# Performance work log

Hardware: AMD Instinct MI355X
Metric: run time of the kernel (lower is better)

## Reference

```python
import jax, jax.numpy as jnp
import numpy as np

B, P, K = 8, 2048, 30   # clouds, points per cloud, kNN neighbors
N = B * P
EPS = 1e-5


def _bn(h, g, b):
    # BatchNorm1d in training mode: batch stats over all non-feature axes (biased var)
    ax = tuple(range(h.ndim - 1))
    m = jnp.mean(h, axis=ax, keepdims=True)
    v = jnp.mean((h - m) ** 2, axis=ax, keepdims=True)
    return g * (h - m) * jax.lax.rsqrt(v + EPS) + b


def _mlp2(x, W0, b0, g0, be0, W1, b1, g1, be1):
    # Seq(Lin, ReLU, BN) x2, matching MLP([cin, 64, 64])
    h = _bn(jax.nn.relu(x @ W0 + b0), g0, be0)
    return _bn(jax.nn.relu(h @ W1 + b1), g1, be1)


def _edgeconv(f, W0, b0, g0, be0, W1, b1, g1, be1):
    # f: [B,P,C]. DynamicEdgeConv: kNN in feature space per cloud (self included,
    # as torch_cluster.knn does), message MLP([x_i, x_j - x_i]), max aggregation.
    s = jnp.sum(f * f, axis=-1)                                   # [B,P]
    d = s[:, :, None] + s[:, None, :] - 2.0 * jnp.einsum('bpc,bqc->bpq', f, f)
    idx = jax.lax.top_k(-d, K)[1]                                  # [B,P,K]
    xj = jax.vmap(lambda ff, ii: ff[ii])(f, idx)                   # [B,P,K,C]
    xi = jnp.broadcast_to(f[:, :, None, :], xj.shape)
    e = jnp.concatenate([xi, xj - xi], axis=-1)                    # [B,P,K,2C]
    return jnp.max(_mlp2(e, W0, b0, g0, be0, W1, b1, g1, be1), axis=2)


def _params():
    key = jax.random.key(1)
    cnt = [0]
    def W(shape, scale=0.05):
        cnt[0] += 1
        return jax.random.normal(jax.random.fold_in(key, cnt[0]), shape, jnp.float32) * scale
    p = {}
    for name, cin in (('c1', 12), ('c2', 128), ('c3', 128)):
        p[name + '_W0'] = W((cin, 64)); p[name + '_b0'] = jnp.zeros(64, jnp.float32)
        p[name + '_g0'] = jnp.ones(64, jnp.float32); p[name + '_be0'] = jnp.zeros(64, jnp.float32)
        p[name + '_W1'] = W((64, 64)); p[name + '_b1'] = jnp.zeros(64, jnp.float32)
        p[name + '_g1'] = jnp.ones(64, jnp.float32); p[name + '_be1'] = jnp.zeros(64, jnp.float32)
    p['l1_W'] = W((192, 1024)); p['l1_b'] = jnp.zeros(1024, jnp.float32)
    p['l1_g'] = jnp.ones(1024, jnp.float32); p['l1_be'] = jnp.zeros(1024, jnp.float32)
    p['h0_W'] = W((1024, 256)); p['h0_b'] = jnp.zeros(256, jnp.float32)
    p['h0_g'] = jnp.ones(256, jnp.float32); p['h0_be'] = jnp.zeros(256, jnp.float32)
    p['h1_W'] = W((256, 128)); p['h1_b'] = jnp.zeros(128, jnp.float32)
    p['h1_g'] = jnp.ones(128, jnp.float32); p['h1_be'] = jnp.zeros(128, jnp.float32)
    p['ho_W'] = W((128, 50)); p['ho_b'] = jnp.zeros(50, jnp.float32)
    return p


def setup_inputs():
    key = jax.random.key(0)
    kx, kp = jax.random.split(key)
    inp = {
        'x': jax.random.normal(kx, (N, 3), jnp.float32),
        'pos': jax.random.normal(kp, (N, 3), jnp.float32),
        'batch': jnp.repeat(jnp.arange(B, dtype=jnp.int32), P),  # B equal-size clouds
    }
    inp.update(_params())
    return inp


def reference(x, pos, batch,
              c1_W0, c1_b0, c1_g0, c1_be0, c1_W1, c1_b1, c1_g1, c1_be1,
              c2_W0, c2_b0, c2_g0, c2_be0, c2_W1, c2_b1, c2_g1, c2_be1,
              c3_W0, c3_b0, c3_g0, c3_be0, c3_W1, c3_b1, c3_g1, c3_be1,
              l1_W, l1_b, l1_g, l1_be,
              h0_W, h0_b, h0_g, h0_be,
              h1_W, h1_b, h1_g, h1_be,
              ho_W, ho_b):
    # batch is assumed to be B equal-sized, sorted clouds -> dense [B,P,C] layout
    f0 = jnp.concatenate([x, pos], axis=-1).reshape(B, P, 6)
    x1 = _edgeconv(f0, c1_W0, c1_b0, c1_g0, c1_be0, c1_W1, c1_b1, c1_g1, c1_be1)
    x2 = _edgeconv(x1, c2_W0, c2_b0, c2_g0, c2_be0, c2_W1, c2_b1, c2_g1, c2_be1)
    x3 = _edgeconv(x2, c3_W0, c3_b0, c3_g0, c3_be0, c3_W1, c3_b1, c3_g1, c3_be1)
    h = jnp.concatenate([x1, x2, x3], axis=-1).reshape(N, 192)
    h = _bn(jax.nn.relu(h @ l1_W + l1_b), l1_g, l1_be)
    h = _bn(jax.nn.relu(h @ h0_W + h0_b), h0_g, h0_be)   # dropout = identity (eval)
    h = _bn(jax.nn.relu(h @ h1_W + h1_b), h1_g, h1_be)
    return jax.nn.log_softmax(h @ ho_W + ho_b, axis=1)
```

## Files before the change

### kernel.cpp

```cpp
#include <hip/hip_runtime.h>
#include <hip/hip_bf16.h>
#include <stdint.h>

#define BNUM 8
#define PNUM 2048
#define KNN  30
#define KSEL 40
#define KCAP 64
#define NPT  (BNUM*PNUM)
#define EPSF 1e-5f

typedef unsigned long long u64;
typedef unsigned short ushort_t;
typedef __attribute__((ext_vector_type(8))) short short8v;
typedef __attribute__((ext_vector_type(4))) float f32x4;

__device__ __forceinline__ unsigned mono_key(float d) {
    unsigned u = __float_as_uint(d);
    return (u & 0x80000000u) ? ~u : (u | 0x80000000u);
}

__device__ __forceinline__ unsigned f2bf(float f) {
    unsigned u = __float_as_uint(f);
    u += 0x7fffu + ((u >> 16) & 1u);
    return u >> 16;
}

__device__ __forceinline__ double lane_bcast64(double x, int l) {
    union { double d; int i[2]; } a; a.d = x;
    union { int i[2]; double d; } r;
    r.i[0] = __builtin_amdgcn_readlane(a.i[0], l);
    r.i[1] = __builtin_amdgcn_readlane(a.i[1], l);
    return r.d;
}

__global__ void k_concat6(const float* __restrict__ x, const float* __restrict__ pos,
                          float* __restrict__ f0) {
    int i = blockIdx.x*256 + threadIdx.x;
    int n = i/6, c = i%6;
    f0[i] = (c < 3) ? x[n*3 + c] : pos[n*3 + c - 3];
}

template<int C>
__global__ __launch_bounds__(256) void k_dist(const float* __restrict__ F,
                                              ushort_t* __restrict__ Dk) {
    __shared__ float FpT[C][132];
    __shared__ float FqT[C][132];
    __shared__ float sp[128], sq[128];
    int b = blockIdx.z;
    int p0 = blockIdx.x*128, q0 = blockIdx.y*128;
    int t = threadIdx.x;
    for (int e = t; e < 128*C; e += 256) {
        int r = e / C, c = e % C;
        FpT[c][r] = F[(size_t)(b*PNUM + p0 + r)*C + c];
        FqT[c][r] = F[(size_t)(b*PNUM + q0 + r)*C + c];
    }
    __syncthreads();
    if (t < 128) {
        float a = 0.f;
        for (int c = 0; c < C; c++) { float xv = FpT[c][t]; a = fmaf(xv, xv, a); }
        sp[t] = a;
    } else {
        int r = t - 128;
        float a = 0.f;
        for (int c = 0; c < C; c++) { float xv = FqT[c][r]; a = fmaf(xv, xv, a); }
        sq[r] = a;
    }
    __syncthreads();
    int tc = (t & 15)*8, tr = (t >> 4)*8;
    float acc[8][8] = {};
    #pragma unroll 4
    for (int c = 0; c < C; c++) {
        float4 p0v = *(const float4*)&FpT[c][tr];
        float4 p1v = *(const float4*)&FpT[c][tr+4];
        float4 q0v = *(const float4*)&FqT[c][tc];
        float4 q1v = *(const float4*)&FqT[c][tc+4];
        float av[8] = {p0v.x,p0v.y,p0v.z,p0v.w,p1v.x,p1v.y,p1v.z,p1v.w};
        float bv[8] = {q0v.x,q0v.y,q0v.z,q0v.w,q1v.x,q1v.y,q1v.z,q1v.w};
        #pragma unroll
        for (int i = 0; i < 8; i++)
            #pragma unroll
            for (int j = 0; j < 8; j++) acc[i][j] = fmaf(av[i], bv[j], acc[i][j]);
    }
    #pragma unroll
    for (int i = 0; i < 8; i++) {
        unsigned ks[8];
        #pragma unroll
        for (int j = 0; j < 8; j++) {
            float d = sp[tr + i] + sq[tc + j] - 2.0f*acc[i][j];
            ks[j] = mono_key(d) >> 16;
        }
        uint4 w;
        w.x = ks[0] | (ks[1] << 16);
        w.y = ks[2] | (ks[3] << 16);
        w.z = ks[4] | (ks[5] << 16);
        w.w = ks[6] | (ks[7] << 16);
        *(uint4*)&Dk[(size_t)(b*PNUM + p0 + tr + i)*PNUM + q0 + tc] = w;
    }
}

__global__ __launch_bounds__(256) void k_topk(const ushort_t* __restrict__ Dk,
                                              int* __restrict__ cand, int* __restrict__ ccnt) {
    __shared__ int red[4];
    __shared__ int wbase[4];
    int n = blockIdx.x, t = threadIdx.x, lane = t & 63, w = t >> 6;
    uint4 wv = *(const uint4*)(Dk + (size_t)n*PNUM + t*8);
    int ks[8];
    ks[0] = wv.x & 0xffff; ks[1] = wv.x >> 16;
    ks[2] = wv.y & 0xffff; ks[3] = wv.y >> 16;
    ks[4] = wv.z & 0xffff; ks[5] = wv.z >> 16;
    ks[6] = wv.w & 0xffff; ks[7] = wv.w >> 16;
    int lo = 0, hi = 65535;
    while (lo < hi) {
        int mid = (lo + hi) >> 1;
        int c = 0;
        #pragma unroll
        for (int e = 0; e < 8; e++) c += (ks[e] <= mid);
        #pragma unroll
        for (int o = 32; o >= 1; o >>= 1) c += __shfl_xor(c, o, 64);
        if (lane == 0) red[w] = c;
        __syncthreads();
        int tot = red[0] + red[1] + red[2] + red[3];
        __syncthreads();
        if (tot >= KSEL) hi = mid; else lo = mid + 1;
    }
    int P = lo;
    int lc = 0;
    #pragma unroll
    for (int e = 0; e < 8; e++) lc += (ks[e] <= P);
    int pre = lc;
    #pragma unroll
    for (int o = 1; o < 64; o <<= 1) { int vv = __shfl_up(pre, o, 64); if (lane >= o) pre += vv; }
    int excl = pre - lc;
    if (lane == 63) red[w] = pre;
    __syncthreads();
    if (t == 0) {
        int s0 = 0;
        #pragma unroll
        for (int i = 0; i < 4; i++) { wbase[i] = s0; s0 += red[i]; }
        ccnt[n] = (s0 < KCAP) ? s0 : KCAP;
    }
    __syncthreads();
    int base = wbase[w] + excl;
    #pragma unroll
    for (int e = 0; e < 8; e++) {
        if (ks[e] <= P) {
            if (base < KCAP) cand[(size_t)n*KCAP + base] = t*8 + e;
            base++;
        }
    }
}

template<int C>
__global__ __launch_bounds__(256) void k_refine(const float* __restrict__ F,
                                                const int* __restrict__ cand,
                                                const int* __restrict__ ccnt,
                                                int* __restrict__ idx) {
    int t = threadIdx.x;
    int lane = t & 63;
    int row = blockIdx.x*4 + (t >> 6);
    int b = row >> 11;
    const float* fp = F + (size_t)row*C;
    int cnt = ccnt[row];
    bool act = lane < cnt;
    int q = act ? cand[(size_t)row*KCAP + lane] : (lane | 0x40000000);
    const float* fq = F + (size_t)(b*PNUM + (act ? q : 0))*C;
    double d = 1e300;
    if (act) {
        d = 0.0;
        if (C == 64) {
            #pragma unroll
            for (int c4 = 0; c4 < C/4; c4++) {
                float4 a = ((const float4*)fp)[c4];
                float4 bb = ((const float4*)fq)[c4];
                double d0 = (double)a.x - (double)bb.x;
                double d1 = (double)a.y - (double)bb.y;
                double d2 = (double)a.z - (double)bb.z;
                double d3 = (double)a.w - (double)bb.w;
                d += d0*d0 + d1*d1 + d2*d2 + d3*d3;
            }
        } else {
            #pragma unroll
            for (int c = 0; c < C; c++) {
                double df = (double)fp[c] - (double)fq[c];
                d += df*df;
            }
        }
    }
    int rank = 0;
    #pragma unroll 16
    for (int l = 0; l < 64; l++) {
        double dl = lane_bcast64(d, l);
        int ql = __builtin_amdgcn_readlane(q, l);
        rank += (dl < d) || (dl == d && ql < q);
    }
    if (act && rank < KNN) idx[(size_t)row*KNN + rank] = q;
}

template<int C>
__global__ __launch_bounds__(256) void k_uv(const float* __restrict__ F,
                                            const float* __restrict__ W0,
                                            const float* __restrict__ b0,
                                            float* __restrict__ u, float* __restrict__ v) {
    __shared__ float As[64][17];
    __shared__ float Wa[16][64];
    __shared__ float Wb[16][64];
    int m0 = blockIdx.x*64;
    int t = threadIdx.x;
    int cb = (t & 15)*4, rb = (t >> 4)*4;
    float aU[4][4] = {}, aV[4][4] = {};
    for (int k0 = 0; k0 < C; k0 += 16) {
        #pragma unroll
        for (int j = 0; j < 4; j++) {
            int e = t + 256*j;
            int r = e >> 4, c = e & 15;
            As[r][c] = (k0 + c < C) ? F[(size_t)(m0 + r)*C + k0 + c] : 0.f;
        }
        {
            int r = t >> 4, c4 = (t & 15)*4;
            bool ok = (k0 + r < C);
            float4 wa = ok ? *(const float4*)&W0[(size_t)(k0 + r)*64 + c4] : make_float4(0,0,0,0);
            float4 wb = ok ? *(const float4*)&W0[(size_t)(C + k0 + r)*64 + c4] : make_float4(0,0,0,0);
            *(float4*)&Wa[r][c4] = wa;
            *(float4*)&Wb[r][c4] = wb;
        }
        __syncthreads();
        #pragma unroll
        for (int kk = 0; kk < 16; kk++) {
            float a[4];
            #pragma unroll
            for (int i = 0; i < 4; i++) a[i] = As[rb + i][kk];
            float4 wa4 = *(const float4*)&Wa[kk][cb];
            float4 wb4 = *(const float4*)&Wb[kk][cb];
            float wa[4] = {wa4.x, wa4.y, wa4.z, wa4.w};
            float wb[4] = {wb4.x, wb4.y, wb4.z, wb4.w};
            #pragma unroll
            for (int i = 0; i < 4; i++)
                #pragma unroll
                for (int j = 0; j < 4; j++) {
                    aU[i][j] = fmaf(a[i], wa[j] - wb[j], aU[i][j]);
                    aV[i][j] = fmaf(a[i], wb[j], aV[i][j]);
                }
        }
        __syncthreads();
    }
    #pragma unroll
    for (int i = 0; i < 4; i++) {
        int row = m0 + rb + i;
        #pragma unroll
        for (int j = 0; j < 4; j++) {
            int col = cb + j;
            u[(size_t)row*64 + col] = aU[i][j] + b0[col];
            v[(size_t)row*64 + col] = aV[i][j];
        }
    }
}

template<int RELU>
__global__ __launch_bounds__(256) void k_gemm(const float* __restrict__ A,
                                              const float* __restrict__ W,
                                              const float* __restrict__ bias,
                                              float* __restrict__ out,
                                              int M, int Kd, int Nd) {
    __shared__ float As[64][17];
    __shared__ float Bs[16][64];
    int m0 = blockIdx.x*64, n0 = blockIdx.y*64;
    int t = threadIdx.x;
    int cb = (t & 15)*4, rb = (t >> 4)*4;
    float acc[4][4] = {};
    for (int k0 = 0; k0 < Kd; k0 += 16) {
        #pragma unroll
        for (int j = 0; j < 4; j++) {
            int e = t + 256*j;
            int r = e >> 4, c = e & 15;
            As[r][c] = (k0 + c < Kd) ? A[(size_t)(m0 + r)*Kd + k0 + c] : 0.f;
        }
        #pragma unroll
        for (int j = 0; j < 4; j++) {
            int e = t + 256*j;
            int r = e >> 6, c = e & 63;
            Bs[r][c] = (k0 + r < Kd && n0 + c < Nd) ? W[(size_t)(k0 + r)*Nd + n0 + c] : 0.f;
        }
        __syncthreads();
        #pragma unroll
        for (int kk = 0; kk < 16; kk++) {
            float a[4];
            #pragma unroll
            for (int i = 0; i < 4; i++) a[i] = As[rb + i][kk];
            float4 w4 = *(const float4*)&Bs[kk][cb];
            float w[4] = {w4.x, w4.y, w4.z, w4.w};
            #pragma unroll
            for (int i = 0; i < 4; i++)
                #pragma unroll
                for (int j = 0; j < 4; j++) acc[i][j] += a[i]*w[j];
        }
        __syncthreads();
    }
    #pragma unroll
    for (int i = 0; i < 4; i++) {
        int row = m0 + rb + i;
        #pragma unroll
        for (int j = 0; j < 4; j++) {
            int col = n0 + cb + j;
            if (col < Nd) {
                float v = acc[i][j] + (bias ? bias[col] : 0.f);
                if (RELU) v = fmaxf(v, 0.f);
                out[(size_t)row*Nd + col] = v;
            }
        }
    }
}

__global__ void k_pack(const float* __restrict__ W, ushort_t* __restrict__ Wpk,
                       int Kd, int Nd) {
    int cell = blockIdx.x*256 + threadIdx.x;
    int ncell = (Kd >> 3)*Nd;
    if (cell >= ncell) return;
    int kg = cell / Nd, n = cell - kg*Nd;
    unsigned b[8];
    #pragma unroll
    for (int j = 0; j < 8; j++) b[j] = f2bf(W[(size_t)(kg*8 + j)*Nd + n]);
    uint4 wv;
    wv.x = b[0] | (b[1] << 16); wv.y = b[2] | (b[3] << 16);
    wv.z = b[4] | (b[5] << 16); wv.w = b[6] | (b[7] << 16);
    *(uint4*)&Wpk[(size_t)cell*8] = wv;
}

template<int CONCAT, int RELU>
__global__ __launch_bounds__(256) void k_mgemm(const float* __restrict__ A,
                                               const float* __restrict__ A2,
                                               const float* __restrict__ A3,
                                               const ushort_t* __restrict__ Wpk,
                                               const float* __restrict__ bias,
                                               float* __restrict__ out,
                                               int Kd, int Nd) {
    __shared__ ushort_t Al[4][128][8];
    __shared__ ushort_t Bl[4][128][8];
    int m0 = blockIdx.x*128, n0 = blockIdx.y*128;
    int t = threadIdx.x, lane = t & 63, w = t >> 6;
    int wm = (w >> 1)*64, wn = (w & 1)*64;
    f32x4 acc[4][4] = {};
    int arow = t >> 2, akg = t & 3;
    for (int k0 = 0; k0 < Kd; k0 += 32) {
        #pragma unroll
        for (int i = 0; i < 2; i++) {
            int row = arow + 64*i;
            int kb = k0 + akg*8;
            const float* src;
            if (CONCAT) {
                const float* s0 = (kb < 64) ? A : (kb < 128) ? A2 : A3;
                src = s0 + (size_t)(m0 + row)*64 + (kb & 63);
            } else {
                src = A + (size_t)(m0 + row)*Kd + kb;
            }
            float4 fa = *(const float4*)src;
            float4 fb = *(const float4*)(src + 4);
            uint4 wv;
            wv.x = f2bf(fa.x) | (f2bf(fa.y) << 16);
            wv.y = f2bf(fa.z) | (f2bf(fa.w) << 16);
            wv.z = f2bf(fb.x) | (f2bf(fb.y) << 16);
            wv.w = f2bf(fb.z) | (f2bf(fb.w) << 16);
            *(uint4*)&Al[akg][row][0] = wv;
        }
        #pragma unroll
        for (int i = 0; i < 2; i++) {
            int cell = t + 256*i;
            int kg = cell >> 7, col = cell & 127;
            *(uint4*)&Bl[kg][col][0] =
                *(const uint4*)&Wpk[((size_t)(k0/8 + kg)*Nd + n0 + col)*8];
        }
        __syncthreads();
        short8v af[4], bf[4];
        #pragma unroll
        for (int mf = 0; mf < 4; mf++)
            af[mf] = *(const short8v*)&Al[lane >> 4][wm + mf*16 + (lane & 15)][0];
        #pragma unroll
        for (int nf = 0; nf < 4; nf++)
            bf[nf] = *(const short8v*)&Bl[lane >> 4][wn + nf*16 + (lane & 15)][0];
        #pragma unroll
        for (int mf = 0; mf < 4; mf++)
            #pragma unroll
            for (int nf = 0; nf < 4; nf++)
                acc[mf][nf] = __builtin_amdgcn_mfma_f32_16x16x32_bf16(af[mf], bf[nf], acc[mf][nf], 0, 0, 0);
        __syncthreads();
    }
    int crow = (lane >> 4)*4;
    int ccol = lane & 15;
    #pragma unroll
    for (int nf = 0; nf < 4; nf++) {
        int col = n0 + wn + nf*16 + ccol;
        float bv = bias[col];
        #pragma unroll
        for (int mf = 0; mf < 4; mf++) {
            #pragma unroll
            for (int r = 0; r < 4; r++) {
                int row = m0 + wm + mf*16 + crow + r;
                float vv = acc[mf][nf][r] + bv;
                if (RELU) vv = fmaxf(vv, 0.f);
                out[(size_t)row*Nd + col] = vv;
            }
        }
    }
}

__global__ __launch_bounds__(256) void k_e1stats(const float* __restrict__ u,
                                                 const float* __restrict__ v,
                                                 const int* __restrict__ idx,
                                                 float* __restrict__ psum, float* __restrict__ psq) {
    int t = threadIdx.x;
    float s0 = 0.f, s1 = 0.f, s2 = 0.f, s3 = 0.f;
    float q0 = 0.f, q1 = 0.f, q2 = 0.f, q3 = 0.f;
    const int stride = 3840*256;
    int i = blockIdx.x*256 + t;
    int c4 = (i & 15)*4;
    #pragma unroll 1
    for (int j = 0; j < 8; j++, i += stride) {
        int edge = i >> 4;
        int p = edge / KNN;
        int q = idx[edge];
        int b = p >> 11;
        float4 uv = *(const float4*)&u[(size_t)p*64 + c4];
        float4 vv = *(const float4*)&v[(size_t)(b*PNUM + q)*64 + c4];
        float h0 = fmaxf(uv.x + vv.x, 0.f);
        float h1 = fmaxf(uv.y + vv.y, 0.f);
        float h2 = fmaxf(uv.z + vv.z, 0.f);
        float h3 = fmaxf(uv.w + vv.w, 0.f);
        s0 += h0; s1 += h1; s2 += h2; s3 += h3;
        q0 = fmaf(h0, h0, q0); q1 = fmaf(h1, h1, q1);
        q2 = fmaf(h2, h2, q2); q3 = fmaf(h3, h3, q3);
    }
    __shared__ float rs[16][16][4];
    __shared__ float rq[16][16][4];
    int slot = t >> 4, g = t & 15;
    rs[slot][g][0] = s0; rs[slot][g][1] = s1; rs[slot][g][2] = s2; rs[slot][g][3] = s3;
    rq[slot][g][0] = q0; rq[slot][g][1] = q1; rq[slot][g][2] = q2; rq[slot][g][3] = q3;
    __syncthreads();
    if (t < 64) {
        int gg = t >> 2, comp = t & 3;
        float ss = 0.f, qq = 0.f;
        #pragma unroll
        for (int sl = 0; sl < 16; sl++) { ss += rs[sl][gg][comp]; qq += rq[sl][gg][comp]; }
        psum[(size_t)blockIdx.x*64 + t] = ss;
        psq [(size_t)blockIdx.x*64 + t] = qq;
    }
}

__global__ void k_statsfin(const float* __restrict__ psum, const float* __restrict__ psq,
                           int npart, int C, float invM,
                           const float* __restrict__ g, const float* __restrict__ be,
                           float* __restrict__ scale, float* __restrict__ shift) {
    int c = blockIdx.x, t = threadIdx.x;
    float s = 0.f, q = 0.f;
    for (int i = t; i < npart; i += 256) {
        s += psum[(size_t)i*C + c];
        q += psq [(size_t)i*C + c];
    }
    __shared__ float rs[256], rq[256];
    rs[t] = s; rq[t] = q; __syncthreads();
    for (int off = 128; off >= 1; off >>= 1) {
        if (t < off) { rs[t] += rs[t+off]; rq[t] += rq[t+off]; }
        __syncthreads();
    }
    if (t == 0) {
        float m   = rs[0]*invM;
        float var = rq[0]*invM - m*m;
        float inv = rsqrtf(var + EPSF);
        float sc  = g[c]*inv;
        scale[c] = sc;
        shift[c] = be[c] - m*sc;
    }
}

__global__ void k_fold(const float* __restrict__ W, const float* __restrict__ b,
                       const float* __restrict__ scale, const float* __restrict__ shift,
                       float* __restrict__ Wp, float* __restrict__ bp, int Cin, int Cout) {
    int co = blockIdx.x, t = threadIdx.x;
    float acc = 0.f;
    for (int ci = t; ci < Cin; ci += 256) {
        float w = W[(size_t)ci*Cout + co];
        Wp[(size_t)ci*Cout + co] = scale[ci]*w;
        acc += shift[ci]*w;
    }
    __shared__ float r[256];
    r[t] = acc; __syncthreads();
    for (int off = 128; off >= 1; off >>= 1) { if (t < off) r[t] += r[t+off]; __syncthreads(); }
    if (t == 0) bp[co] = b[co] + r[0];
}

__global__ __launch_bounds__(256, 4) void k_e2(const float* __restrict__ u, const float* __restrict__ v,
                                               const int* __restrict__ idx,
                                               const float* __restrict__ W1p, const float* __restrict__ b1p,
                                               float* __restrict__ pmax, float* __restrict__ pmin,
                                               float* __restrict__ psum, float* __restrict__ psq) {
    __shared__ float hbuf[4][64];
    int t = threadIdx.x, lane = t & 63, w = t >> 6;
    int p = blockIdx.x*4 + w;
    int b = p >> 11;
    float wcol[64];
    #pragma unroll
    for (int c = 0; c < 64; c++) wcol[c] = W1p[c*64 + lane];
    #pragma unroll
    for (int c = 0; c < 64; c++) asm volatile("" : "+v"(wcol[c]));
    float ureg = u[(size_t)p*64 + lane];
    float bias = b1p[lane];
    const int* myidx = idx + (size_t)p*KNN;
    const float* vb = v + (size_t)b*PNUM*64;
    float mx = -1e30f, mn = 1e30f, sm = 0.f, sq = 0.f;
    int q = myidx[0];
    float vk = vb[(size_t)q*64 + lane];
    #pragma unroll 1
    for (int k = 0; k < KNN; k++) {
        float h = fmaxf(ureg + vk, 0.f);
        hbuf[w][lane] = h;
        if (k + 1 < KNN) {
            int qn = myidx[k + 1];
            vk = vb[(size_t)qn*64 + lane];
        }
        float a0 = 0.f, a1 = 0.f, a2 = 0.f, a3 = 0.f;
        #pragma unroll
        for (int c = 0; c < 64; c += 4) {
            float4 h4 = *(const float4*)&hbuf[w][c];
            a0 = fmaf(h4.x, wcol[c    ], a0);
            a1 = fmaf(h4.y, wcol[c + 1], a1);
            a2 = fmaf(h4.z, wcol[c + 2], a2);
            a3 = fmaf(h4.w, wcol[c + 3], a3);
        }
        float o = fmaxf((a0 + a1) + (a2 + a3) + bias, 0.f);
        mx = fmaxf(mx, o);
        mn = fminf(mn, o);
        sm += o;
        sq = fmaf(o, o, sq);
    }
    pmax[(size_t)p*64 + lane] = mx;
    pmin[(size_t)p*64 + lane] = mn;
    psum[(size_t)p*64 + lane] = sm;
    psq [(size_t)p*64 + lane] = sq;
}

__global__ void k_applypool(const float* __restrict__ pmax, const float* __restrict__ pmin,
                            const float* __restrict__ scale, const float* __restrict__ shift,
                            float* __restrict__ out) {
    int i = blockIdx.x*256 + threadIdx.x;
    int c = i & 63;
    float sc = scale[c];
    float pooled = (sc >= 0.f) ? pmax[i] : pmin[i];
    out[i] = sc*pooled + shift[c];
}

__global__ void k_colstats(const float* __restrict__ Hbuf, float* __restrict__ psum,
                           float* __restrict__ psq, int Cout) {
    int m0 = blockIdx.x*64, c0 = blockIdx.y*64;
    int t = threadIdx.x;
    int c = t & 63, rg = t >> 6;
    float s = 0.f, q = 0.f;
    #pragma unroll 4
    for (int r = 0; r < 16; r++) {
        float hv = Hbuf[(size_t)(m0 + rg*16 + r)*Cout + c0 + c];
        s += hv; q += hv*hv;
    }
    __shared__ float rs[256], rq[256];
    rs[t] = s; rq[t] = q; __syncthreads();
    if (t < 128) { rs[t] += rs[t+128]; rq[t] += rq[t+128]; }
    __syncthreads();
    if (t < 64) {
        rs[t] += rs[t+64]; rq[t] += rq[t+64];
        psum[(size_t)blockIdx.x*Cout + c0 + t] = rs[t];
        psq [(size_t)blockIdx.x*Cout + c0 + t] = rq[t];
    }
}

__global__ void k_logsoftmax(const float* __restrict__ logits, float* __restrict__ out) {
    int t = threadIdx.x;
    int n = blockIdx.x*4 + (t >> 6);
    int l = t & 63;
    float z = (l < 50) ? logits[(size_t)n*50 + l] : -INFINITY;
    float mx = z;
    #pragma unroll
    for (int off = 32; off >= 1; off >>= 1) mx = fmaxf(mx, __shfl_xor(mx, off, 64));
    float ex = (l < 50) ? expf(z - mx) : 0.f;
    float sm = ex;
    #pragma unroll
    for (int off = 32; off >= 1; off >>= 1) sm += __shfl_xor(sm, off, 64);
    float lse = mx + logf(sm);
    if (l < 50) out[(size_t)n*50 + l] = z - lse;
}

extern "C" void kernel_launch(void* const* d_in, const int* in_sizes, int n_in,
                              void* d_out, int out_size, void* d_ws, size_t ws_size,
                              hipStream_t stream) {
    (void)in_sizes; (void)n_in; (void)out_size;
    const float* x   = (const float*)d_in[0];
    const float* pos = (const float*)d_in[1];
    const float* prm[38];
    for (int i = 0; i < 38; i++) prm[i] = (const float*)d_in[3 + i];

    float* ws = (float*)d_ws;
    size_t off = 0;
    auto alloc = [&](size_t cnt) { float* p = ws + off; off += (cnt + 63) & ~((size_t)63); return p; };
    float* f0   = alloc((size_t)NPT*6);
    float* x1   = alloc((size_t)NPT*64);
    float* x2   = alloc((size_t)NPT*64);
    float* x3   = alloc((size_t)NPT*64);
    float* u    = alloc((size_t)NPT*64);
    float* v    = alloc((size_t)NPT*64);
    float* pmax = alloc((size_t)NPT*64);
    float* pmin = alloc((size_t)NPT*64);
    int*   idx  = (int*)alloc((size_t)NPT*KNN);
    int*   ccnt = (int*)alloc(NPT);
    float* W1p  = alloc(64*64);
    float* b1p  = alloc(64);
    float* scaleA = alloc(1024);
    float* shiftA = alloc(1024);
    float* Wp   = alloc(1024*256);
    float* bp   = alloc(1024);
    ushort_t* Wpk1 = (ushort_t*)alloc(98304);
    ushort_t* Wpk2 = (ushort_t*)alloc(131072);
    float* psum = alloc((size_t)NPT*64);
    float* psq  = alloc((size_t)NPT*64);
    float* big  = alloc((size_t)BNUM*PNUM*PNUM);
    if (off*sizeof(float) > ws_size) return;

    int* cand = (int*)psum;
    ushort_t* Dk = (ushort_t*)big;

    auto conv = [&](const float* F, int C, const float* const* pp, float* xout) {
        if (C == 6) k_dist<6><<<dim3(16,16,8), 256, 0, stream>>>(F, Dk);
        else        k_dist<64><<<dim3(16,16,8), 256, 0, stream>>>(F, Dk);
        k_topk<<<NPT, 256, 0, stream>>>(Dk, cand, ccnt);
        if (C == 6) k_refine<6><<<NPT/4, 256, 0, stream>>>(F, cand, ccnt, idx);
        else        k_refine<64><<<NPT/4, 256, 0, stream>>>(F, cand, ccnt, idx);
        if (C == 6) k_uv<6><<<NPT/64, 256, 0, stream>>>(F, pp[0], pp[1], u, v);
        else        k_uv<64><<<NPT/64, 256, 0, stream>>>(F, pp[0], pp[1], u, v);
        k_e1stats<<<3840, 256, 0, stream>>>(u, v, idx, psum, psq);
        k_statsfin<<<64, 256, 0, stream>>>(psum, psq, 3840, 64, 1.f/((float)NPT*KNN),
                                           pp[2], pp[3], scaleA, shiftA);
        k_fold<<<64, 256, 0, stream>>>(pp[4], pp[5], scaleA, shiftA, W1p, b1p, 64, 64);
        k_e2<<<NPT/4, 256, 0, stream>>>(u, v, idx, W1p, b1p, pmax, pmin, psum, psq);
        k_statsfin<<<64, 256, 0, stream>>>(psum, psq, NPT, 64, 1.f/((float)NPT*KNN),
                                           pp[6], pp[7], scaleA, shiftA);
        k_applypool<<<NPT*64/256, 256, 0, stream>>>(pmax, pmin, scaleA, shiftA, xout);
    };

    k_concat6<<<NPT*6/256, 256, 0, stream>>>(x, pos, f0);
    k_pack<<<96, 256, 0, stream>>>(prm[24], Wpk1, 192, 1024);
    conv(f0, 6,  &prm[0],  x1);
    conv(x1, 64, &prm[8],  x2);
    conv(x2, 64, &prm[16], x3);

    float* Hb1    = big + 3145728;
    float* Hb2    = big + 19922944;
    float* Hb3    = big + 24117248;
    float* logits = big + 26214400;

    k_mgemm<1,1><<<dim3(NPT/128, 8), 256, 0, stream>>>(x1, x2, x3, Wpk1, prm[25], Hb1, 192, 1024);
    k_colstats<<<dim3(NPT/64, 16), 256, 0, stream>>>(Hb1, psum, psq, 1024);
    k_statsfin<<<1024, 256, 0, stream>>>(psum, psq, NPT/64, 1024, 1.f/(float)NPT,
                                         prm[26], prm[27], scaleA, shiftA);
    k_fold<<<256, 256, 0, stream>>>(prm[28], prm[29], scaleA, shiftA, Wp, bp, 1024, 256);
    k_pack<<<128, 256, 0, stream>>>(Wp, Wpk2, 1024, 256);
    k_mgemm<0,1><<<dim3(NPT/128, 2), 256, 0, stream>>>(Hb1, nullptr, nullptr, Wpk2, bp, Hb2, 1024, 256);
    k_colstats<<<dim3(NPT/64, 4), 256, 0, stream>>>(Hb2, psum, psq, 256);
    k_statsfin<<<256, 256, 0, stream>>>(psum, psq, NPT/64, 256, 1.f/(float)NPT,
                                        prm[30], prm[31], scaleA, shiftA);
    k_fold<<<128, 256, 0, stream>>>(prm[32], prm[33], scaleA, shiftA, Wp, bp, 256, 128);
    k_pack<<<16, 256, 0, stream>>>(Wp, Wpk2, 256, 128);
    k_mgemm<0,1><<<dim3(NPT/128, 1), 256, 0, stream>>>(Hb2, nullptr, nullptr, Wpk2, bp, Hb3, 256, 128);
    k_colstats<<<dim3(NPT/64, 2), 256, 0, stream>>>(Hb3, psum, psq, 128);
    k_statsfin<<<128, 256, 0, stream>>>(psum, psq, NPT/64, 128, 1.f/(float)NPT,
                                        prm[34], prm[35], scaleA, shiftA);
    k_fold<<<50, 256, 0, stream>>>(prm[36], prm[37], scaleA, shiftA, Wp, bp, 128, 50);
    k_gemm<0><<<dim3(NPT/64, 1), 256, 0, stream>>>(Hb3, Wp, bp, logits, NPT, 128, 50);
    k_logsoftmax<<<NPT/4, 256, 0, stream>>>(logits, (float*)d_out);
}
```

Baseline: 1.145 ms.

## Restructure edge MLP second layer as tiled register-blocked GEMM per 4 points

The second-layer edge kernel used to give each wave one point and loop over 30 neighbours, doing a 64x64 matvec per neighbour out of LDS. It now treats 4 points x 32 neighbour slots as a 128x64 tile and stages the gathered, ReLU'd hidden rows and W1 through shared memory in K-chunks of 16. Each thread computes an 8x8 output block, and pooling and stats are reduced through LDS at the end. This raises FMA-to-load ratio and reuses weights across rows, at the cost of padding two unused neighbour slots per point, more barriers, and heavier register use per thread.

```diff
diff --git a/kernel.cpp b/kernel.cpp
--- a/kernel.cpp
+++ b/kernel.cpp
@@ -487,54 +487,114 @@
     if (t == 0) bp[co] = b[co] + r[0];
 }
 
-__global__ __launch_bounds__(256, 4) void k_e2(const float* __restrict__ u, const float* __restrict__ v,
-                                               const int* __restrict__ idx,
-                                               const float* __restrict__ W1p, const float* __restrict__ b1p,
-                                               float* __restrict__ pmax, float* __restrict__ pmin,
-                                               float* __restrict__ psum, float* __restrict__ psq) {
-    __shared__ float hbuf[4][64];
-    int t = threadIdx.x, lane = t & 63, w = t >> 6;
-    int p = blockIdx.x*4 + w;
-    int b = p >> 11;
-    float wcol[64];
-    #pragma unroll
-    for (int c = 0; c < 64; c++) wcol[c] = W1p[c*64 + lane];
-    #pragma unroll
-    for (int c = 0; c < 64; c++) asm volatile("" : "+v"(wcol[c]));
-    float ureg = u[(size_t)p*64 + lane];
-    float bias = b1p[lane];
-    const int* myidx = idx + (size_t)p*KNN;
-    const float* vb = v + (size_t)b*PNUM*64;
-    float mx = -1e30f, mn = 1e30f, sm = 0.f, sq = 0.f;
-    int q = myidx[0];
-    float vk = vb[(size_t)q*64 + lane];
-    #pragma unroll 1
-    for (int k = 0; k < KNN; k++) {
-        float h = fmaxf(ureg + vk, 0.f);
-        hbuf[w][lane] = h;
-        if (k + 1 < KNN) {
-            int qn = myidx[k + 1];
-            vk = vb[(size_t)qn*64 + lane];
-        }
-        float a0 = 0.f, a1 = 0.f, a2 = 0.f, a3 = 0.f;
-        #pragma unroll
-        for (int c = 0; c < 64; c += 4) {
-            float4 h4 = *(const float4*)&hbuf[w][c];
-            a0 = fmaf(h4.x, wcol[c    ], a0);
-            a1 = fmaf(h4.y, wcol[c + 1], a1);
-            a2 = fmaf(h4.z, wcol[c + 2], a2);
-            a3 = fmaf(h4.w, wcol[c + 3], a3);
-        }
-        float o = fmaxf((a0 + a1) + (a2 + a3) + bias, 0.f);
-        mx = fmaxf(mx, o);
-        mn = fminf(mn, o);
-        sm += o;
-        sq = fmaf(o, o, sq);
-    }
-    pmax[(size_t)p*64 + lane] = mx;
-    pmin[(size_t)p*64 + lane] = mn;
-    psum[(size_t)p*64 + lane] = sm;
-    psq [(size_t)p*64 + lane] = sq;
+__global__ __launch_bounds__(128) void k_e2(const float* __restrict__ u, const float* __restrict__ v,
+                                            const int* __restrict__ idx,
+                                            const float* __restrict__ W1p, const float* __restrict__ b1p,
+                                            float* __restrict__ pmax, float* __restrict__ pmin,
+                                            float* __restrict__ psum, float* __restrict__ psq) {
+    __shared__ float As[16][132];
+    __shared__ float Bs[16][68];
+    __shared__ float us[4][64];
+    __shared__ int   qs[128];
+    __shared__ float pool[4][16][68];
+    int t = threadIdx.x;
+    int p0 = blockIdx.x*4;
+    int bb = p0 >> 11;
+    {
+        int r = t;
+        int k = r & 31, pt = r >> 5;
+        qs[r] = (k < KNN) ? idx[(size_t)(p0 + pt)*KNN + k] : -1;
+    }
+    for (int e = t; e < 256; e += 128)
+        us[e >> 6][e & 63] = u[(size_t)(p0 + (e >> 6))*64 + (e & 63)];
+    __syncthreads();
+    int tc = (t & 7)*8, tr = (t >> 3)*8;
+    float acc[8][8] = {};
+    const float* vb = v + (size_t)bb*PNUM*64;
+    for (int k0 = 0; k0 < 64; k0 += 16) {
+        #pragma unroll
+        for (int i = 0; i < 2; i++) {
+            int cell = t + 128*i;
+            int r = cell >> 4, c4 = (cell & 15)*4;
+            *(float4*)&Bs[r][c4] = *(const float4*)&W1p[(size_t)(k0 + r)*64 + c4];
+        }
+        #pragma unroll
+        for (int i = 0; i < 4; i++) {
+            int cell = t + 128*i;
+            int r = cell >> 2, g = cell & 3;
+            int q = qs[r];
+            float4 h4 = make_float4(0.f, 0.f, 0.f, 0.f);
+            if (q >= 0) {
+                float4 u4 = *(const float4*)&us[r >> 5][k0 + g*4];
+                float4 v4 = *(const float4*)&vb[(size_t)q*64 + k0 + g*4];
+                h4.x = fmaxf(u4.x + v4.x, 0.f);
+                h4.y = fmaxf(u4.y + v4.y, 0.f);
+                h4.z = fmaxf(u4.z + v4.z, 0.f);
+                h4.w = fmaxf(u4.w + v4.w, 0.f);
+            }
+            As[g*4+0][r] = h4.x; As[g*4+1][r] = h4.y;
+            As[g*4+2][r] = h4.z; As[g*4+3][r] = h4.w;
+        }
+        __syncthreads();
+        #pragma unroll
+        for (int kk = 0; kk < 16; kk++) {
+            float4 a0 = *(const float4*)&As[kk][tr];
+            float4 a1 = *(const float4*)&As[kk][tr+4];
+            float4 b0 = *(const float4*)&Bs[kk][tc];
+            float4 b1 = *(const float4*)&Bs[kk][tc+4];
+            float av[8] = {a0.x,a0.y,a0.z,a0.w,a1.x,a1.y,a1.z,a1.w};
+            float bv[8] = {b0.x,b0.y,b0.z,b0.w,b1.x,b1.y,b1.z,b1.w};
+            #pragma unroll
+            for (int i = 0; i < 8; i++)
+                #pragma unroll
+                for (int j = 0; j < 8; j++) acc[i][j] = fmaf(av[i], bv[j], acc[i][j]);
+        }
+        __syncthreads();
+    }
+    float bj[8];
+    #pragma unroll
+    for (int j = 0; j < 8; j++) bj[j] = b1p[tc + j];
+    float mx[8], mn[8], sm[8], sq[8];
+    #pragma unroll
+    for (int j = 0; j < 8; j++) { mx[j] = -1e30f; mn[j] = 1e30f; sm[j] = 0.f; sq[j] = 0.f; }
+    #pragma unroll
+    for (int i = 0; i < 8; i++) {
+        int k = (tr + i) & 31;
+        if (k < KNN) {
+            #pragma unroll
+            for (int j = 0; j < 8; j++) {
+                float o = fmaxf(acc[i][j] + bj[j], 0.f);
+                mx[j] = fmaxf(mx[j], o);
+                mn[j] = fminf(mn[j], o);
+                sm[j] += o;
+                sq[j] = fmaf(o, o, sq[j]);
+            }
+        }
+    }
+    int rg = t >> 3;
+    #pragma unroll
+    for (int j = 0; j < 8; j++) {
+        pool[0][rg][tc+j] = mx[j];
+        pool[1][rg][tc+j] = mn[j];
+        pool[2][rg][tc+j] = sm[j];
+        pool[3][rg][tc+j] = sq[j];
+    }
+    __syncthreads();
+    for (int e = t; e < 256; e += 128) {
+        int pt = e >> 6, co = e & 63;
+        float m0 = -1e30f, m1 = 1e30f, s0 = 0.f, s1 = 0.f;
+        #pragma unroll
+        for (int b2 = 0; b2 < 4; b2++) {
+            m0 = fmaxf(m0, pool[0][pt*4+b2][co]);
+            m1 = fminf(m1, pool[1][pt*4+b2][co]);
+            s0 += pool[2][pt*4+b2][co];
+            s1 += pool[3][pt*4+b2][co];
+        }
+        pmax[(size_t)(p0+pt)*64 + co] = m0;
+        pmin[(size_t)(p0+pt)*64 + co] = m1;
+        psum[(size_t)(p0+pt)*64 + co] = s0;
+        psq [(size_t)(p0+pt)*64 + co] = s1;
+    }
 }
 
 __global__ void k_applypool(const float* __restrict__ pmax, const float* __restrict__ pmin,
@@ -635,7 +695,7 @@
         k_statsfin<<<64, 256, 0, stream>>>(psum, psq, 3840, 64, 1.f/((float)NPT*KNN),
                                            pp[2], pp[3], scaleA, shiftA);
         k_fold<<<64, 256, 0, stream>>>(pp[4], pp[5], scaleA, shiftA, W1p, b1p, 64, 64);
-        k_e2<<<NPT/4, 256, 0, stream>>>(u, v, idx, W1p, b1p, pmax, pmin, psum, psq);
+        k_e2<<<NPT/4, 128, 0, stream>>>(u, v, idx, W1p, b1p, pmax, pmin, psum, psq);
         k_statsfin<<<64, 256, 0, stream>>>(psum, psq, NPT, 64, 1.f/((float)NPT*KNN),
                                            pp[6], pp[7], scaleA, shiftA);
         k_applypool<<<NPT*64/256, 256, 0, stream>>>(pmax, pmin, scaleA, shiftA, xout);
```

New measurement: 1.223 ms. 1.07x slower.

## Compute 64-channel kNN distance matrix with bf16 MFMA instead of FP32 FMA

Applied to the files above, without the earlier changes.

For the 64-channel edge convolutions, the pairwise distance Gram matrix is now computed with bf16 MFMA 16x16x32 instructions on tiles staged in shared memory, replacing the scalar FP32 8x8 register-tile loop. Squared norms are computed in FP32 by a separate small kernel. The bf16 dot products lose precision, which the later FP32 refine stage over an oversized candidate set is expected to absorb. The output stores are now scalar 16-bit writes instead of packed uint4 stores, and an unroll pragma was removed from the FP32 kernel.

```diff
diff --git a/kernel.cpp b/kernel.cpp
--- a/kernel.cpp
+++ b/kernel.cpp
@@ -39,6 +39,14 @@
     int i = blockIdx.x*256 + threadIdx.x;
     int n = i/6, c = i%6;
     f0[i] = (c < 3) ? x[n*3 + c] : pos[n*3 + c - 3];
+}
+
+template<int C>
+__global__ void k_snorm(const float* __restrict__ F, float* __restrict__ s) {
+    int n = blockIdx.x*256 + threadIdx.x;
+    float a = 0.f;
+    for (int c = 0; c < C; c++) { float t = F[(size_t)n*C + c]; a = fmaf(t, t, a); }
+    s[n] = a;
 }
 
 template<int C>
@@ -69,7 +77,6 @@
     __syncthreads();
     int tc = (t & 15)*8, tr = (t >> 4)*8;
     float acc[8][8] = {};
-    #pragma unroll 4
     for (int c = 0; c < C; c++) {
         float4 p0v = *(const float4*)&FpT[c][tr];
         float4 p1v = *(const float4*)&FpT[c][tr+4];
@@ -96,6 +103,79 @@
         w.z = ks[4] | (ks[5] << 16);
         w.w = ks[6] | (ks[7] << 16);
         *(uint4*)&Dk[(size_t)(b*PNUM + p0 + tr + i)*PNUM + q0 + tc] = w;
+    }
+}
+
+__global__ __launch_bounds__(256) void k_mdist(const float* __restrict__ F,
+                                               const float* __restrict__ s,
+                                               ushort_t* __restrict__ Dk) {
+    __shared__ ushort_t Ap[8][128][8];
+    __shared__ ushort_t Aq[8][128][8];
+    __shared__ float sp[128], sq[128];
+    int b = blockIdx.z;
+    int p0 = blockIdx.x*128, q0 = blockIdx.y*128;
+    int t = threadIdx.x, lane = t & 63, w = t >> 6;
+    int wm = (w >> 1)*64, wn = (w & 1)*64;
+    if (t < 128) sp[t] = s[b*PNUM + p0 + t];
+    else         sq[t-128] = s[b*PNUM + q0 + (t-128)];
+    #pragma unroll
+    for (int it = 0; it < 4; it++) {
+        int cell = t + 256*it;
+        int row = cell >> 3, kg = cell & 7;
+        {
+            const float* src = &F[(size_t)(b*PNUM + p0 + row)*64 + kg*8];
+            float4 fa = *(const float4*)src, fb = *(const float4*)(src + 4);
+            uint4 wv;
+            wv.x = f2bf(fa.x) | (f2bf(fa.y) << 16);
+            wv.y = f2bf(fa.z) | (f2bf(fa.w) << 16);
+            wv.z = f2bf(fb.x) | (f2bf(fb.y) << 16);
+            wv.w = f2bf(fb.z) | (f2bf(fb.w) << 16);
+            *(uint4*)&Ap[kg][row][0] = wv;
+        }
+        {
+            const float* src = &F[(size_t)(b*PNUM + q0 + row)*64 + kg*8];
+            float4 fa = *(const float4*)src, fb = *(const float4*)(src + 4);
+            uint4 wv;
+            wv.x = f2bf(fa.x) | (f2bf(fa.y) << 16);
+            wv.y = f2bf(fa.z) | (f2bf(fa.w) << 16);
+            wv.z = f2bf(fb.x) | (f2bf(fb.y) << 16);
+            wv.w = f2bf(fb.z) | (f2bf(fb.w) << 16);
+            *(uint4*)&Aq[kg][row][0] = wv;
+        }
+    }
+    __syncthreads();
+    f32x4 acc[4][4] = {};
+    #pragma unroll
+    for (int ks = 0; ks < 2; ks++) {
+        short8v af[4], bf[4];
+        #pragma unroll
+        for (int mf = 0; mf < 4; mf++)
+            af[mf] = *(const short8v*)&Ap[ks*4 + (lane >> 4)][wm + mf*16 + (lane & 15)][0];
+        #pragma unroll
+        for (int nf = 0; nf < 4; nf++)
+            bf[nf] = *(const short8v*)&Aq[ks*4 + (lane >> 4)][wn + nf*16 + (lane & 15)][0];
+        #pragma unroll
+        for (int mf = 0; mf < 4; mf++)
+            #pragma unroll
+            for (int nf = 0; nf < 4; nf++)
+                acc[mf][nf] = __builtin_amdgcn_mfma_f32_16x16x32_bf16(af[mf], bf[nf], acc[mf][nf], 0, 0, 0);
+    }
+    int crow = (lane >> 4)*4;
+    int ccol = lane & 15;
+    #pragma unroll
+    for (int mf = 0; mf < 4; mf++) {
+        #pragma unroll
+        for (int r = 0; r < 4; r++) {
+            int row = wm + mf*16 + crow + r;
+            float spv = sp[row];
+            size_t base = (size_t)(b*PNUM + p0 + row)*PNUM + q0;
+            #pragma unroll
+            for (int nf = 0; nf < 4; nf++) {
+                int col = wn + nf*16 + ccol;
+                float d = spv + sq[col] - 2.0f*acc[mf][nf][r];
+                Dk[base + col] = (ushort_t)(mono_key(d) >> 16);
+            }
+        }
     }
 }
 
@@ -598,6 +678,7 @@
     size_t off = 0;
     auto alloc = [&](size_t cnt) { float* p = ws + off; off += (cnt + 63) & ~((size_t)63); return p; };
     float* f0   = alloc((size_t)NPT*6);
+    float* s    = alloc(NPT);
     float* x1   = alloc((size_t)NPT*64);
     float* x2   = alloc((size_t)NPT*64);
     float* x3   = alloc((size_t)NPT*64);
@@ -624,8 +705,12 @@
     ushort_t* Dk = (ushort_t*)big;
 
     auto conv = [&](const float* F, int C, const float* const* pp, float* xout) {
-        if (C == 6) k_dist<6><<<dim3(16,16,8), 256, 0, stream>>>(F, Dk);
-        else        k_dist<64><<<dim3(16,16,8), 256, 0, stream>>>(F, Dk);
+        if (C == 6) {
+            k_dist<6><<<dim3(16,16,8), 256, 0, stream>>>(F, Dk);
+        } else {
+            k_snorm<64><<<NPT/256, 256, 0, stream>>>(F, s);
+            k_mdist<<<dim3(16,16,8), 256, 0, stream>>>(F, s, Dk);
+        }
         k_topk<<<NPT, 256, 0, stream>>>(Dk, cand, ccnt);
         if (C == 6) k_refine<6><<<NPT/4, 256, 0, stream>>>(F, cand, ccnt, idx);
         else        k_refine<64><<<NPT/4, 256, 0, stream>>>(F, cand, ccnt, idx);
```

Measured after the change: 1.070 ms. 1.07x faster.
